# Performance work log

Measured on AMD Instinct MI355X. Metric: run time of the kernel, lower is better.

## Reference

```python
import jax, jax.numpy as jnp
import numpy as np

N_INST, BATCH, IN_DIM, L_DIM = 256, 128, 1024, 512

def setup_inputs() -> dict:
    key = jax.random.key(0)
    k1, k2, k3, k4 = jax.random.split(key, 4)
    # glorot-uniform-ish scales
    sv = np.sqrt(6.0 / (IN_DIM + L_DIM)).astype(np.float32)
    sw = np.sqrt(6.0 / (L_DIM + 1)).astype(np.float32)
    x = jax.random.normal(k1, (N_INST, BATCH, IN_DIM), dtype=jnp.float32)
    v = jax.random.uniform(k2, (IN_DIM, L_DIM), minval=-sv, maxval=sv, dtype=jnp.float32)
    u = jax.random.uniform(k3, (IN_DIM, L_DIM), minval=-sv, maxval=sv, dtype=jnp.float32)
    w = jax.random.uniform(k4, (L_DIM, 1), minval=-sw, maxval=sw, dtype=jnp.float32)
    return {"x": x, "v": v, "u": u, "w": w}

def reference(x, v, u, w):
    # x: [n_instances, batch, in_dim]
    # Fused batched version of the per-instance loop:
    # score_i = (tanh(x_i @ v) * sigmoid(x_i @ u)) @ w, softmax over instances.
    h = jnp.tanh(jnp.einsum('nbd,dl->nbl', x, v))          # [n, b, l]
    g = jax.nn.sigmoid(jnp.einsum('nbd,dl->nbl', x, u))    # [n, b, l]
    scores = jnp.einsum('nbl,lo->nbo', h * g, w)            # [n, b, 1]
    alpha = jax.nn.softmax(scores, axis=0)                  # softmax over instance axis
    return alpha
```

## Files before the change

### kernel.cpp

```cpp
#include <hip/hip_runtime.h>
#include <stdint.h>

typedef unsigned int  u32;
typedef unsigned short u16;
typedef __bf16 v8bf __attribute__((ext_vector_type(8)));
typedef float  v4f  __attribute__((ext_vector_type(4)));

#define N_INST 256
#define BATCH  128
#define IN_DIM 1024
#define L_DIM  512
#define M_TOT  (N_INST*BATCH)
#define NSLICE 16

#define XB_BYTES   ((size_t)M_TOT * IN_DIM * 2)
#define WPK_BYTES  ((size_t)1024 * IN_DIM * 2)

__device__ inline u32 f2bf_pk(float a, float b){
  u32 ua = __builtin_bit_cast(u32, a);
  u32 ub = __builtin_bit_cast(u32, b);
  ua = (ua + 0x7FFFu + ((ua >> 16) & 1u)) >> 16;
  ub = (ub + 0x7FFFu + ((ub >> 16) & 1u)) & 0xFFFF0000u;
  return ua | ub;
}

__device__ inline void gl2lds16(const u16* g, u16* l){
  __builtin_amdgcn_global_load_lds(
      (const __attribute__((address_space(1))) u32*)(g),
      (__attribute__((address_space(3))) u32*)(l), 16, 0, 0);
}

#define PREP_XBLKS 16384
__global__ void prep(const float* __restrict__ x, const float* __restrict__ v,
                     const float* __restrict__ u, u16* __restrict__ xb,
                     u16* __restrict__ wpk){
  const int b = blockIdx.x;
  if (b < PREP_XBLKS){
    int t = b * 256 + threadIdx.x;
    int r = t >> 6, l = t & 63;
    int kk = r & 1, i = (r >> 1) & 3, h = (r >> 3) & 1, kt = (r >> 4) & 15, mb = r >> 8;
    int q = l >> 4, c = l & 15;
    int row = mb*128 + h*64 + i*16 + c;
    int k0  = kt*64 + kk*32 + q*8;
    const float* src = x + (size_t)row * IN_DIM + k0;
    float4 a0 = *reinterpret_cast<const float4*>(src);
    float4 a1 = *reinterpret_cast<const float4*>(src + 4);
    uint4 out;
    out.x = f2bf_pk(a0.x, a0.y); out.y = f2bf_pk(a0.z, a0.w);
    out.z = f2bf_pk(a1.x, a1.y); out.w = f2bf_pk(a1.z, a1.w);
    *reinterpret_cast<uint4*>(xb + (size_t)r*512 + l*8) = out;
  } else {
    int t = (b - PREP_XBLKS) * 256 + threadIdx.x;
    int r = t >> 6, l = t & 63;
    int kk = r & 1, j = (r >> 1) & 3, kt = (r >> 3) & 15, cs = r >> 7;
    int q = l >> 4, c = l & 15;
    int bcol = cs*4 + j;
    const float* src = (bcol & 1) ? u : v;
    int lcol = (bcol >> 1)*16 + c;
    int k0 = kt*64 + kk*32 + q*8;
    u32 o[4];
#pragma unroll
    for (int ii = 0; ii < 4; ++ii){
      float a  = src[(size_t)(k0 + 2*ii    ) * L_DIM + lcol];
      float bb = src[(size_t)(k0 + 2*ii + 1) * L_DIM + lcol];
      o[ii] = f2bf_pk(a, bb);
    }
    *reinterpret_cast<uint4*>(wpk + (size_t)r*512 + l*8) = make_uint4(o[0], o[1], o[2], o[3]);
  }
}


#define STAGE(KT, LB) { _Pragma("unroll") for (int it_ = 0; it_ < 6; ++it_)           \
    gl2lds16(sp[it_] + (size_t)(KT)*sstr[it_], &Ls[(LB) + (wave*6+it_)*512]); }

#define LOADA_F(P, LB, KK) { _Pragma("unroll") for (int gi_ = 0; gi_ < 4; ++gi_)      \
    afb[P][gi_] = *reinterpret_cast<const v8bf*>(&Ls[(LB) + ao0 + (gi_*2+(KK))*512]); }

#define LOADB_F(P, LB, KK) { _Pragma("unroll") for (int j_ = 0; j_ < 4; ++j_)         \
    bfb[P][j_] = *reinterpret_cast<const v8bf*>(&Ls[(LB) + bo0 + (j_*2+(KK))*512]); }

#define STEPX(P, DO_R, LB, NKK) {                                                     \
  __builtin_amdgcn_s_setprio(1);                                                      \
  _Pragma("unroll") for (int j_ = 0; j_ < 4; ++j_){                                   \
    _Pragma("unroll") for (int gi_ = 0; gi_ < 4; ++gi_)                               \
      acc[gi_][j_] = __builtin_amdgcn_mfma_f32_16x16x32_bf16(                         \
          afb[P][gi_], bfb[P][j_], acc[gi_][j_], 0, 0, 0);                            \
    if (DO_R) bfb[(P)^1][j_] = *reinterpret_cast<const v8bf*>(                        \
        &Ls[(LB) + bo0 + (j_*2+(NKK))*512]);                                          \
  }                                                                                   \
  __builtin_amdgcn_s_setprio(0);                                                      \
  if (DO_R) LOADA_F((P)^1, LB, NKK); }

#define WAIT_BAR {                                                                    \
  __builtin_amdgcn_sched_barrier(0);                                                  \
  asm volatile("s_waitcnt vmcnt(0)" ::: "memory");                                    \
  __builtin_amdgcn_s_barrier();                                                       \
  __builtin_amdgcn_sched_barrier(0); }

__launch_bounds__(512, 2)
__global__ void gemm_score(const u16* __restrict__ xb, const u16* __restrict__ wpk,
                           const float* __restrict__ w, float* __restrict__ partial){
  __shared__ __align__(16) u16 Ls[2*48*512];

  const int tid  = threadIdx.x;
  const u32 bid  = blockIdx.x;
  const int lo  = bid & 7;
  const int csp = (bid >> 3) & 7;
  const int hi  = bid >> 6;
  const int m   = lo*16 + hi;
  const int mblk0 = m*2;

  const int lane = tid & 63;
  const int wave = tid >> 6;
  const int q    = lane >> 4;
  const int c    = lane & 15;
  const int wm   = wave >> 1;
  const int wn   = wave & 1;

  const u16* sp[6]; u32 sstr[6];
#pragma unroll
  for (int it = 0; it < 6; ++it){
    int r = wave*6 + it;
    if (r < 32){
      sp[it]   = xb + ((size_t)(mblk0 + (r>>4))*256 + (r&15))*512 + lane*8;
      sstr[it] = 16*512;
    } else {
      int rb = r - 32;
      sp[it]   = wpk + ((size_t)((csp*2 + (rb>>3))*128 + (rb&7)))*512 + lane*8;
      sstr[it] = 8*512;
    }
  }

  const u32 ao0 = (u32)(((wm>>1)*16 + (wm&1)*8)*512) + lane*8;
  const u32 bo0 = (u32)((32 + wn*8)*512) + lane*8;

  v8bf afb[2][4];
  v8bf bfb[2][4];
  v4f  acc[4][4];
#pragma unroll
  for (int gi = 0; gi < 4; ++gi)
#pragma unroll
    for (int j = 0; j < 4; ++j)
      acc[gi][j] = (v4f){0.f, 0.f, 0.f, 0.f};

  STAGE(0, 0);
  u32 lb = 0;

#pragma unroll 1
  for (int kt = 0; kt < 16; ++kt){
    WAIT_BAR;
    if (kt < 15) STAGE(kt+1, lb ^ 24576);
    LOADA_F(0, lb, 0); LOADB_F(0, lb, 0);
    STEPX(0, 1, lb, 1);
    STEPX(1, 0, lb, 0);
    lb ^= 24576;
  }

  const int cs = csp*2 + wn;
  const float wl0 = w[cs*32 + c];
  const float wl1 = w[cs*32 + 16 + c];
  float* pout = partial + (size_t)cs * M_TOT + (size_t)m*256 + wm*64;

#pragma unroll
  for (int gi = 0; gi < 4; ++gi){
#pragma unroll
    for (int r = 0; r < 4; ++r){
      float t0 = 2.f / (1.f + __expf(-2.f * acc[gi][0][r])) - 1.f;
      float s0 = 1.f / (1.f + __expf(-acc[gi][1][r]));
      float t1 = 2.f / (1.f + __expf(-2.f * acc[gi][2][r])) - 1.f;
      float s1 = 1.f / (1.f + __expf(-acc[gi][3][r]));
      float v2 = t0*s0*wl0 + t1*s1*wl1;
      v2 += __shfl_xor(v2, 1, 64);
      v2 += __shfl_xor(v2, 2, 64);
      v2 += __shfl_xor(v2, 4, 64);
      v2 += __shfl_xor(v2, 8, 64);
      if (c == 0) pout[gi*16 + q*4 + r] = v2;
    }
  }
}

__global__ void softmax_inst(const float* __restrict__ partial, float* __restrict__ out){
  __shared__ float red[N_INST];
  const int b = blockIdx.x;
  const int n = threadIdx.x;
  float s = 0.f;
#pragma unroll
  for (int i = 0; i < NSLICE; ++i) s += partial[(size_t)i * M_TOT + n*BATCH + b];
  red[n] = s; __syncthreads();
  for (int st = N_INST/2; st > 0; st >>= 1){
    if (n < st) red[n] = fmaxf(red[n], red[n + st]);
    __syncthreads();
  }
  float mx = red[0]; __syncthreads();
  float e = __expf(s - mx);
  red[n] = e; __syncthreads();
  for (int st = N_INST/2; st > 0; st >>= 1){
    if (n < st) red[n] += red[n + st];
    __syncthreads();
  }
  out[n*BATCH + b] = e / red[0];
}

extern "C" void kernel_launch(void* const* d_in, const int* in_sizes, int n_in,
                              void* d_out, int out_size, void* d_ws, size_t ws_size,
                              hipStream_t stream) {
  const float* x = (const float*)d_in[0];
  const float* v = (const float*)d_in[1];
  const float* u = (const float*)d_in[2];
  const float* w = (const float*)d_in[3];
  u16*   xb      = (u16*)d_ws;
  u16*   wpk     = (u16*)((char*)d_ws + XB_BYTES);
  float* partial = (float*)((char*)d_ws + XB_BYTES + WPK_BYTES);
  float* out     = (float*)d_out;

  prep<<<dim3(PREP_XBLKS + 512), dim3(256), 0, stream>>>(x, v, u, xb, wpk);
  gemm_score<<<dim3(1024), dim3(512), 0, stream>>>(xb, wpk, w, partial);
  softmax_inst<<<dim3(BATCH), dim3(N_INST), 0, stream>>>(partial, out);
}
```

Baseline: 292.4 us.

## Switch GEMM to triple-buffered half-K LDS stages with partial vmcnt waits

Splits each 64-wide K tile into two 32-wide sub-stages and rotates three smaller LDS buffers, waiting only for the oldest in-flight loads (vmcnt(3)) instead of draining all loads before each barrier. The LDS footprint per block drops, and launch bounds are raised to allow four blocks per CU, aiming for better latency hiding and occupancy. The cost is twice as many barriers, the loss of register double-buffering of fragments, and tighter register budgets at the higher occupancy target.

```diff
diff --git a/kernel.cpp b/kernel.cpp
--- a/kernel.cpp
+++ b/kernel.cpp
@@ -70,37 +70,36 @@
 }
 
 
-#define STAGE(KT, LB) { _Pragma("unroll") for (int it_ = 0; it_ < 6; ++it_)           \
-    gl2lds16(sp[it_] + (size_t)(KT)*sstr[it_], &Ls[(LB) + (wave*6+it_)*512]); }
-
-#define LOADA_F(P, LB, KK) { _Pragma("unroll") for (int gi_ = 0; gi_ < 4; ++gi_)      \
-    afb[P][gi_] = *reinterpret_cast<const v8bf*>(&Ls[(LB) + ao0 + (gi_*2+(KK))*512]); }
-
-#define LOADB_F(P, LB, KK) { _Pragma("unroll") for (int j_ = 0; j_ < 4; ++j_)         \
-    bfb[P][j_] = *reinterpret_cast<const v8bf*>(&Ls[(LB) + bo0 + (j_*2+(KK))*512]); }
-
-#define STEPX(P, DO_R, LB, NKK) {                                                     \
+#define STAGE_P(KKC, RB) { _Pragma("unroll") for (int it_ = 0; it_ < 3; ++it_)        \
+    gl2lds16(sp[it_] + (KKC)*512, &Ls[(RB) + (wave3 + it_)*512]); }
+
+#define STAGE_N(KKC, RB) { _Pragma("unroll") for (int it_ = 0; it_ < 3; ++it_)        \
+    gl2lds16(sp[it_] + sstr[it_] + (KKC)*512, &Ls[(RB) + (wave3 + it_)*512]); }
+
+#define FRAGS(RB) {                                                                   \
+  _Pragma("unroll") for (int gi_ = 0; gi_ < 4; ++gi_)                                 \
+    afb[gi_] = *reinterpret_cast<const v8bf*>(&Ls[(RB) + ao0 + gi_*512]);             \
+  _Pragma("unroll") for (int j_ = 0; j_ < 4; ++j_)                                    \
+    bfb[j_] = *reinterpret_cast<const v8bf*>(&Ls[(RB) + bo0 + j_*512]); }
+
+#define MFMA16 {                                                                      \
   __builtin_amdgcn_s_setprio(1);                                                      \
-  _Pragma("unroll") for (int j_ = 0; j_ < 4; ++j_){                                   \
+  _Pragma("unroll") for (int j_ = 0; j_ < 4; ++j_)                                    \
     _Pragma("unroll") for (int gi_ = 0; gi_ < 4; ++gi_)                               \
       acc[gi_][j_] = __builtin_amdgcn_mfma_f32_16x16x32_bf16(                         \
-          afb[P][gi_], bfb[P][j_], acc[gi_][j_], 0, 0, 0);                            \
-    if (DO_R) bfb[(P)^1][j_] = *reinterpret_cast<const v8bf*>(                        \
-        &Ls[(LB) + bo0 + (j_*2+(NKK))*512]);                                          \
-  }                                                                                   \
-  __builtin_amdgcn_s_setprio(0);                                                      \
-  if (DO_R) LOADA_F((P)^1, LB, NKK); }
-
-#define WAIT_BAR {                                                                    \
+          afb[gi_], bfb[j_], acc[gi_][j_], 0, 0, 0);                                  \
+  __builtin_amdgcn_s_setprio(0); }
+
+#define BARC(N) {                                                                     \
   __builtin_amdgcn_sched_barrier(0);                                                  \
-  asm volatile("s_waitcnt vmcnt(0)" ::: "memory");                                    \
+  asm volatile("s_waitcnt vmcnt(" #N ")" ::: "memory");                               \
   __builtin_amdgcn_s_barrier();                                                       \
   __builtin_amdgcn_sched_barrier(0); }
 
-__launch_bounds__(512, 2)
+__launch_bounds__(512, 4)
 __global__ void gemm_score(const u16* __restrict__ xb, const u16* __restrict__ wpk,
                            const float* __restrict__ w, float* __restrict__ partial){
-  __shared__ __align__(16) u16 Ls[2*48*512];
+  __shared__ __align__(16) u16 Ls[3*24*512];
 
   const int tid  = threadIdx.x;
   const u32 bid  = blockIdx.x;
@@ -112,30 +111,31 @@
 
   const int lane = tid & 63;
   const int wave = tid >> 6;
+  const int wave3= wave*3;
   const int q    = lane >> 4;
   const int c    = lane & 15;
   const int wm   = wave >> 1;
   const int wn   = wave & 1;
 
-  const u16* sp[6]; u32 sstr[6];
-#pragma unroll
-  for (int it = 0; it < 6; ++it){
-    int r = wave*6 + it;
-    if (r < 32){
-      sp[it]   = xb + ((size_t)(mblk0 + (r>>4))*256 + (r&15))*512 + lane*8;
+  const u16* sp[3]; u32 sstr[3];
+#pragma unroll
+  for (int it = 0; it < 3; ++it){
+    int r = wave3 + it;
+    if (r < 16){
+      sp[it]   = xb + ((size_t)(mblk0 + (r>>3))*256 + (r&7)*2)*512 + lane*8;
       sstr[it] = 16*512;
     } else {
-      int rb = r - 32;
-      sp[it]   = wpk + ((size_t)((csp*2 + (rb>>3))*128 + (rb&7)))*512 + lane*8;
+      int rb_ = r - 16;
+      sp[it]   = wpk + ((size_t)((csp*2 + (rb_>>2))*128 + (rb_&3)*2))*512 + lane*8;
       sstr[it] = 8*512;
     }
   }
 
-  const u32 ao0 = (u32)(((wm>>1)*16 + (wm&1)*8)*512) + lane*8;
-  const u32 bo0 = (u32)((32 + wn*8)*512) + lane*8;
-
-  v8bf afb[2][4];
-  v8bf bfb[2][4];
+  const u32 ao0 = (u32)(((wm>>1)*8 + (wm&1)*4)*512) + lane*8;
+  const u32 bo0 = (u32)((16 + wn*4)*512) + lane*8;
+
+  v8bf afb[4];
+  v8bf bfb[4];
   v4f  acc[4][4];
 #pragma unroll
   for (int gi = 0; gi < 4; ++gi)
@@ -143,18 +143,31 @@
     for (int j = 0; j < 4; ++j)
       acc[gi][j] = (v4f){0.f, 0.f, 0.f, 0.f};
 
-  STAGE(0, 0);
-  u32 lb = 0;
+  u32 rb0 = 0, rb1 = 12288, rb2 = 24576;
+
+  STAGE_P(0, rb0);
+  STAGE_P(1, rb1);
+  BARC(3);
 
 #pragma unroll 1
-  for (int kt = 0; kt < 16; ++kt){
-    WAIT_BAR;
-    if (kt < 15) STAGE(kt+1, lb ^ 24576);
-    LOADA_F(0, lb, 0); LOADB_F(0, lb, 0);
-    STEPX(0, 1, lb, 1);
-    STEPX(1, 0, lb, 0);
-    lb ^= 24576;
-  }
+  for (int kt = 0; kt < 15; ++kt){
+    STAGE_N(0, rb2);
+    FRAGS(rb0);
+    MFMA16;
+    BARC(3);
+    STAGE_N(1, rb0);
+    FRAGS(rb1);
+    MFMA16;
+    BARC(3);
+    { u32 t = rb0; rb0 = rb2; rb2 = rb1; rb1 = t; }
+#pragma unroll
+    for (int it = 0; it < 3; ++it) sp[it] += sstr[it];
+  }
+  FRAGS(rb0);
+  MFMA16;
+  BARC(0);
+  FRAGS(rb1);
+  MFMA16;
 
   const int cs = csp*2 + wn;
   const float wl0 = w[cs*32 + c];
```

Result: no change. 288.1 us (-1.5%).
